# Optimization experiments

Hardware: AMD Instinct MI355X
Metric: run time of the kernel (lower is better)

Reference implementation:

```python
import jax, jax.numpy as jnp
import numpy as np

B, H, W, C = 32, 56, 56, 512
WS, SHIFT, NH = 7, 3, 16
HID = 4 * C
EPS = 1e-5


def layernorm(x, g, b):
    m = jnp.mean(x, axis=-1, keepdims=True)
    v = jnp.mean(jnp.square(x - m), axis=-1, keepdims=True)
    return (x - m) * jax.lax.rsqrt(v + EPS) * g + b


def setup_inputs() -> dict:
    key = jax.random.key(0)
    ks = jax.random.split(key, 16)
    s = 0.02
    return {
        "x": jax.random.normal(ks[0], (B, H * W, C), jnp.float32),
        "wqkv": jax.random.normal(ks[1], (3 * C, C), jnp.float32) * s,
        "bqkv": jnp.zeros((3 * C,), jnp.float32),
        "wo": jax.random.normal(ks[2], (C, C), jnp.float32) * s,
        "bo": jnp.zeros((C,), jnp.float32),
        "g1": jnp.ones((C,), jnp.float32),
        "b1": jnp.zeros((C,), jnp.float32),
        "g2": jnp.ones((C,), jnp.float32),
        "b2": jnp.zeros((C,), jnp.float32),
        "w_mlp1": jax.random.normal(ks[3], (HID, C), jnp.float32) * s,
        "b_mlp1": jnp.zeros((HID,), jnp.float32),
        "w_mlp2": jax.random.normal(ks[4], (C, HID), jnp.float32) * s,
        "b_mlp2": jnp.zeros((C,), jnp.float32),
    }


def window_partition(x4):
    # (B,H,W,C) -> (B*nW, WS*WS, C)
    x = x4.reshape(B, H // WS, WS, W // WS, WS, C)
    return x.transpose(0, 1, 3, 2, 4, 5).reshape(-1, WS * WS, C)


def window_reverse(win):
    # (B*nW, WS*WS, C) -> (B,H,W,C)
    x = win.reshape(B, H // WS, W // WS, WS, WS, C)
    return x.transpose(0, 1, 3, 2, 4, 5).reshape(B, H, W, C)


def mha(xn, wqkv, bqkv, wo, bo):
    NW, T, _ = xn.shape
    Dh = C // NH
    qkv = xn @ wqkv.T + bqkv                      # (NW, T, 3C)
    q, k, v = jnp.split(qkv, 3, axis=-1)
    sh = lambda t: t.reshape(NW, T, NH, Dh).transpose(0, 2, 1, 3)  # (NW,NH,T,Dh)
    q, k, v = sh(q), sh(k), sh(v)
    scores = jnp.einsum('whqd,whkd->whqk', q, k) * (Dh ** -0.5)
    a = jax.nn.softmax(scores, axis=-1)
    o = jnp.einsum('whqk,whkd->whqd', a, v).transpose(0, 2, 1, 3).reshape(NW, T, C)
    return o @ wo.T + bo


def reference(x, wqkv, bqkv, wo, bo, g1, b1, g2, b2, w_mlp1, b_mlp1, w_mlp2, b_mlp2):
    x4 = x.reshape(B, H, W, C)
    shifted = jnp.roll(x4, (-SHIFT, -SHIFT), axis=(1, 2))
    win = window_partition(shifted)               # (B*64, 49, C)
    shortcut = win
    wn = layernorm(win, g1, b1)
    attn = mha(wn, wqkv, bqkv, wo, bo)
    win = shortcut + attn
    _ = window_reverse(win)  # NOTE: discarded, faithfully matching the source (x is rebuilt from shifted_x)
    xr = jnp.roll(shifted, (SHIFT, SHIFT), axis=(1, 2)).reshape(B, H * W, C)
    h = layernorm(xr, g2, b2)
    h = jax.nn.gelu(h @ w_mlp1.T + b_mlp1, approximate=False) @ w_mlp2.T + b_mlp2
    return xr + h
```

## Files before the change

kernel.cpp:

```cpp
#include <hip/hip_runtime.h>
#include <hip/hip_bf16.h>
#include <cstdint>
#include <cstddef>

#define MROWS 100352
#define CDIM  512
#define HDIM  2048

typedef __attribute__((ext_vector_type(8))) short   short8;
typedef __attribute__((ext_vector_type(8))) __bf16  bf16x8;
typedef __attribute__((ext_vector_type(4))) __bf16  bf16x4;
typedef __attribute__((ext_vector_type(4))) float   floatx4;

static __device__ __forceinline__ unsigned short f2bf(float f) {
  union { float f; unsigned int u; } c; c.f = f;
  unsigned int u = c.u;
  return (unsigned short)((u + 0x7FFFu + ((u >> 16) & 1u)) >> 16);
}

static __device__ __forceinline__ void gload_lds16(const void* g, void* l) {
  __builtin_amdgcn_global_load_lds(
      (const __attribute__((address_space(1))) void*)g,
      (__attribute__((address_space(3))) void*)l, 16, 0, 0);
}

#define BAR()   asm volatile("s_barrier" ::: "memory")
#define LGKM0() asm volatile("s_waitcnt lgkmcnt(0)" ::: "memory")
#define VMC4()  asm volatile("s_waitcnt vmcnt(4)" ::: "memory")
#define VMC0()  asm volatile("s_waitcnt vmcnt(0)" ::: "memory")

__global__ void cast_weights(const float4* __restrict__ s1, unsigned short* __restrict__ d1,
                             const float4* __restrict__ s2, unsigned short* __restrict__ d2) {
  int t = blockIdx.x * 256 + threadIdx.x;
  const int N4 = (HDIM * CDIM) / 4;
  const float4* s; unsigned short* d; int idx;
  if (t < N4) { s = s1; d = d1; idx = t; }
  else        { s = s2; d = d2; idx = t - N4; }
  float4 f = s[idx];
  ushort4 u = make_ushort4(f2bf(f.x), f2bf(f.y), f2bf(f.z), f2bf(f.w));
  *reinterpret_cast<ushort4*>(d + (size_t)idx * 4) = u;
}

__global__ void ln_cast(const float* __restrict__ x, const float* __restrict__ g,
                        const float* __restrict__ b, unsigned short* __restrict__ xn) {
  const int row  = blockIdx.x * 4 + (threadIdx.x >> 6);
  const int lane = threadIdx.x & 63;
  const float4* xr = reinterpret_cast<const float4*>(x + (size_t)row * CDIM);
  const float4 v0 = xr[lane], v1 = xr[lane + 64];
  float s  = v0.x + v0.y + v0.z + v0.w + v1.x + v1.y + v1.z + v1.w;
  float ss = v0.x*v0.x + v0.y*v0.y + v0.z*v0.z + v0.w*v0.w
           + v1.x*v1.x + v1.y*v1.y + v1.z*v1.z + v1.w*v1.w;
#pragma unroll
  for (int o = 1; o < 64; o <<= 1) { s += __shfl_xor(s, o); ss += __shfl_xor(ss, o); }
  const float mean = s * (1.0f / CDIM);
  const float rstd = rsqrtf(ss * (1.0f / CDIM) - mean * mean + 1e-5f);
  const float4* g4 = reinterpret_cast<const float4*>(g);
  const float4* b4 = reinterpret_cast<const float4*>(b);
  const float4 ga = g4[lane], gb = g4[lane + 64];
  const float4 ba = b4[lane], bb = b4[lane + 64];
  ushort4 o0 = make_ushort4(
      f2bf((v0.x - mean) * rstd * ga.x + ba.x),
      f2bf((v0.y - mean) * rstd * ga.y + ba.y),
      f2bf((v0.z - mean) * rstd * ga.z + ba.z),
      f2bf((v0.w - mean) * rstd * ga.w + ba.w));
  ushort4 o1 = make_ushort4(
      f2bf((v1.x - mean) * rstd * gb.x + bb.x),
      f2bf((v1.y - mean) * rstd * gb.y + bb.y),
      f2bf((v1.z - mean) * rstd * gb.z + bb.z),
      f2bf((v1.w - mean) * rstd * gb.w + bb.w));
  unsigned short* orow = xn + (size_t)row * CDIM;
  *reinterpret_cast<ushort4*>(orow + lane * 4)        = o0;
  *reinterpret_cast<ushort4*>(orow + (lane + 64) * 4) = o1;
}

template<int KDIM, int NDIM, int EPI>
__global__ __launch_bounds__(512, 2) void gemm256(
    const unsigned short* __restrict__ A, const unsigned short* __restrict__ Bw,
    const float* __restrict__ bias, const float* __restrict__ resid,
    void* __restrict__ Cout) {
  __shared__ __align__(16) unsigned short sm[2][2][2][8192];

  const int tid  = threadIdx.x;
  const int lane = tid & 63, w = tid >> 6;
  const int swr = w >> 2, swc = w & 3;
  const int frow = tid & 15, fk = ((tid & 63) >> 4) * 8;

  constexpr int GX = NDIM / 256;
  const int nwg = gridDim.x;
  const int lid = ((int)blockIdx.x & 7) * (nwg >> 3) + ((int)blockIdx.x >> 3);
  const int m0 = (lid / GX) * 256, n0 = (lid % GX) * 256;

  const size_t ldb = (size_t)KDIM * 2;
  const int srow = tid >> 3;
  const int scb  = ((tid ^ (tid >> 3)) & 7) * 16;
  const char* gA = (const char*)A  + (size_t)(m0 + srow) * ldb + scb;
  const char* gB = (const char*)Bw + (size_t)(n0 + srow) * ldb + scb;

  auto STG = [&](const char* gbase, int tile, int half, int isB) {
    unsigned short* hb = &sm[isB][tile & 1][half][0];
    const char* s = gbase + (size_t)half * 128 * ldb + (size_t)tile * 128;
    gload_lds16(s,            hb + w * 512);
    gload_lds16(s + 64 * ldb, hb + 4096 + w * 512);
  };
  auto LDA = [&](bf16x8* a, int db, int qm) {
#pragma unroll
    for (int mi = 0; mi < 4; ++mi)
#pragma unroll
      for (int kk = 0; kk < 2; ++kk) {
        const int row = swr * 64 + mi * 16 + frow;
        const int col = kk * 32 + fk;
        const int sidx = row * 64 + (col ^ ((row & 7) << 3));
        a[mi * 2 + kk] = __builtin_bit_cast(bf16x8,
            *reinterpret_cast<const short8*>(&sm[0][db][qm][sidx]));
      }
  };
  auto LDBf = [&](bf16x8* b, int db, int qn) {
#pragma unroll
    for (int nj = 0; nj < 2; ++nj)
#pragma unroll
      for (int kk = 0; kk < 2; ++kk) {
        const int row = swc * 32 + nj * 16 + frow;
        const int col = kk * 32 + fk;
        const int sidx = row * 64 + (col ^ ((row & 7) << 3));
        b[nj * 2 + kk] = __builtin_bit_cast(bf16x8,
            *reinterpret_cast<const short8*>(&sm[1][db][qn][sidx]));
      }
  };

  floatx4 acc[2][2][4][2] = {};
  auto MM = [&](floatx4 (*a2)[2], const bf16x8* a, const bf16x8* b) {
    __builtin_amdgcn_s_setprio(1);
#pragma unroll
    for (int mi = 0; mi < 4; ++mi)
#pragma unroll
      for (int nj = 0; nj < 2; ++nj)
#pragma unroll
        for (int kk = 0; kk < 2; ++kk)
          a2[mi][nj] = __builtin_amdgcn_mfma_f32_16x16x32_bf16(
              b[nj * 2 + kk], a[mi * 2 + kk], a2[mi][nj], 0, 0, 0);
    __builtin_amdgcn_s_setprio(0);
  };

  constexpr int nt = KDIM / 64;

  STG(gA, 0, 0, 0); STG(gB, 0, 0, 1);
  STG(gA, 0, 1, 0); STG(gB, 0, 1, 1);
  STG(gA, 1, 0, 0); STG(gB, 1, 0, 1);
  VMC4();
  BAR();

  for (int t2 = 0; t2 < nt; ++t2) {
    const int db = t2 & 1;
    bf16x8 a[8], b0[4], b1[4];

    LDA(a, db, 0); LDBf(b0, db, 0);
    if (t2 + 1 < nt) STG(gA, t2 + 1, 1, 0);
    BAR(); LGKM0();
    MM(acc[0][0], a, b0);
    BAR();

    LDBf(b1, db, 1);
    if (t2 + 1 < nt) STG(gB, t2 + 1, 1, 1);
    BAR(); LGKM0();
    MM(acc[0][1], a, b1);
    BAR();

    LDA(a, db, 1);
    if (t2 + 2 < nt) STG(gA, t2 + 2, 0, 0);
    BAR(); LGKM0();
    MM(acc[1][0], a, b0);
    BAR();

    if (t2 + 2 < nt) STG(gB, t2 + 2, 0, 1);
    BAR(); LGKM0();
    MM(acc[1][1], a, b1);
    if (t2 < nt - 2)       { VMC4(); }
    else if (t2 == nt - 2) { VMC0(); }
    BAR();
  }

  const int em = lane & 15;
  const int en = (lane >> 4) << 2;

  float4 bj[4];
#pragma unroll
  for (int qn = 0; qn < 2; ++qn)
#pragma unroll
    for (int nj = 0; nj < 2; ++nj)
      bj[qn * 2 + nj] = *reinterpret_cast<const float4*>(
          &bias[n0 + qn * 128 + swc * 32 + nj * 16 + en]);

#pragma unroll
  for (int qm = 0; qm < 2; ++qm)
#pragma unroll
    for (int mi = 0; mi < 4; ++mi) {
      const int gm = m0 + qm * 128 + swr * 64 + mi * 16 + em;
      const size_t rowoff = (size_t)gm * NDIM + n0 + swc * 32 + en;
#pragma unroll
      for (int qn = 0; qn < 2; ++qn)
#pragma unroll
        for (int nj = 0; nj < 2; ++nj) {
          const float4 bb = bj[qn * 2 + nj];
          const floatx4 av = acc[qm][qn][mi][nj];
          float v0 = av[0] + bb.x, v1 = av[1] + bb.y;
          float v2 = av[2] + bb.z, v3 = av[3] + bb.w;
          const size_t off = rowoff + qn * 128 + nj * 16;
          if (EPI == 1) {
            v0 *= __builtin_amdgcn_rcpf(1.0f + __expf(-1.702f * v0));
            v1 *= __builtin_amdgcn_rcpf(1.0f + __expf(-1.702f * v1));
            v2 *= __builtin_amdgcn_rcpf(1.0f + __expf(-1.702f * v2));
            v3 *= __builtin_amdgcn_rcpf(1.0f + __expf(-1.702f * v3));
            bf16x4 o = { (__bf16)v0, (__bf16)v1, (__bf16)v2, (__bf16)v3 };
            *reinterpret_cast<bf16x4*>((unsigned short*)Cout + off) = o;
          } else {
            const float4 r4 = *reinterpret_cast<const float4*>(resid + off);
            float4 o = make_float4(v0 + r4.x, v1 + r4.y, v2 + r4.z, v3 + r4.w);
            *reinterpret_cast<float4*>((float*)Cout + off) = o;
          }
        }
    }
}

extern "C" void kernel_launch(void* const* d_in, const int* in_sizes, int n_in,
                              void* d_out, int out_size, void* d_ws, size_t ws_size,
                              hipStream_t stream) {
  const float* x   = (const float*)d_in[0];
  const float* g2  = (const float*)d_in[7];
  const float* b2  = (const float*)d_in[8];
  const float* w1  = (const float*)d_in[9];
  const float* b1  = (const float*)d_in[10];
  const float* w2  = (const float*)d_in[11];
  const float* b2m = (const float*)d_in[12];
  float* out = (float*)d_out;


  unsigned short* w1b = (unsigned short*)d_ws;
  unsigned short* w2b = w1b + (size_t)HDIM * CDIM;
  unsigned short* G   = w2b + (size_t)HDIM * CDIM;
  unsigned short* xn = (unsigned short*)d_out;

  cast_weights<<<2048, 256, 0, stream>>>((const float4*)w1, w1b, (const float4*)w2, w2b);
  ln_cast<<<MROWS / 4, 256, 0, stream>>>(x, g2, b2, xn);

  gemm256<CDIM, HDIM, 1><<<dim3((HDIM / 256) * (MROWS / 256)), 512, 0, stream>>>(
      xn, w1b, b1, nullptr, (void*)G);
  gemm256<HDIM, CDIM, 2><<<dim3((CDIM / 256) * (MROWS / 256)), 512, 0, stream>>>(
      G, w2b, b2m, x, (void*)out);
}
```

Baseline: 643.8 us.

## Replace quarter-split GEMM pipeline with simple double-buffered templated tile kernel

Swaps the hand-interleaved four-quadrant GEMM schedule, which had staged loads, barriers and partial vmcnt waits, for a plain double-buffered loop. Each iteration prefetches the next full K-tile and computes the current one, then waits for all loads and syncs once. The kernel is now templated on BN and the warp grid, and the second GEMM uses 256x128 tiles with a 4x2 warp layout, doubling its workgroup count. The simpler schedule drops the fine-grained overlap and needs more registers for larger fragment sets, in exchange for fewer barriers.

```diff
diff --git a/kernel.cpp b/kernel.cpp
--- a/kernel.cpp
+++ b/kernel.cpp
@@ -25,8 +25,6 @@
 }
 
 #define BAR()   asm volatile("s_barrier" ::: "memory")
-#define LGKM0() asm volatile("s_waitcnt lgkmcnt(0)" ::: "memory")
-#define VMC4()  asm volatile("s_waitcnt vmcnt(4)" ::: "memory")
 #define VMC0()  asm volatile("s_waitcnt vmcnt(0)" ::: "memory")
 
 __global__ void cast_weights(const float4* __restrict__ s1, unsigned short* __restrict__ d1,
@@ -73,22 +71,30 @@
   *reinterpret_cast<ushort4*>(orow + (lane + 64) * 4) = o1;
 }
 
-template<int KDIM, int NDIM, int EPI>
-__global__ __launch_bounds__(512, 2) void gemm256(
+template<int KDIM, int NDIM, int BN, int WGM, int WGN, int EPI>
+__global__ __launch_bounds__(512, 2) void gemm_pipe(
     const unsigned short* __restrict__ A, const unsigned short* __restrict__ Bw,
     const float* __restrict__ bias, const float* __restrict__ resid,
     void* __restrict__ Cout) {
-  __shared__ __align__(16) unsigned short sm[2][2][2][8192];
+  constexpr int BM   = 256;
+  constexpr int WM   = BM / WGM;
+  constexpr int WN   = BN / WGN;
+  constexpr int AM16 = WM / 16;
+  constexpr int AN16 = WN / 16;
+  constexpr int nt   = KDIM / 64;
+
+  __shared__ __align__(16) unsigned short smA[2][BM * 64];
+  __shared__ __align__(16) unsigned short smB[2][BN * 64];
 
   const int tid  = threadIdx.x;
   const int lane = tid & 63, w = tid >> 6;
-  const int swr = w >> 2, swc = w & 3;
-  const int frow = tid & 15, fk = ((tid & 63) >> 4) * 8;
-
-  constexpr int GX = NDIM / 256;
+  const int swr = w / WGN, swc = w % WGN;
+  const int frow = lane & 15, fk = (lane >> 4) * 8;
+
+  constexpr int GX = NDIM / BN;
   const int nwg = gridDim.x;
   const int lid = ((int)blockIdx.x & 7) * (nwg >> 3) + ((int)blockIdx.x >> 3);
-  const int m0 = (lid / GX) * 256, n0 = (lid % GX) * 256;
+  const int m0 = (lid / GX) * BM, n0 = (lid % GX) * BN;
 
   const size_t ldb = (size_t)KDIM * 2;
   const int srow = tid >> 3;
@@ -96,129 +102,100 @@
   const char* gA = (const char*)A  + (size_t)(m0 + srow) * ldb + scb;
   const char* gB = (const char*)Bw + (size_t)(n0 + srow) * ldb + scb;
 
-  auto STG = [&](const char* gbase, int tile, int half, int isB) {
-    unsigned short* hb = &sm[isB][tile & 1][half][0];
-    const char* s = gbase + (size_t)half * 128 * ldb + (size_t)tile * 128;
-    gload_lds16(s,            hb + w * 512);
-    gload_lds16(s + 64 * ldb, hb + 4096 + w * 512);
+  auto STG = [&](int t, int buf) {
+    const char* sa = gA + (size_t)t * 128;
+    const char* sb = gB + (size_t)t * 128;
+#pragma unroll
+    for (int j = 0; j < BM / 64; ++j)
+      gload_lds16(sa + (size_t)j * 64 * ldb, &smA[buf][j * 4096 + w * 512]);
+#pragma unroll
+    for (int j = 0; j < BN / 64; ++j)
+      gload_lds16(sb + (size_t)j * 64 * ldb, &smB[buf][j * 4096 + w * 512]);
   };
-  auto LDA = [&](bf16x8* a, int db, int qm) {
-#pragma unroll
-    for (int mi = 0; mi < 4; ++mi)
+
+  floatx4 acc[AM16][AN16] = {};
+
+  STG(0, 0);
+  VMC0();
+  BAR();
+
+  for (int t = 0; t < nt; ++t) {
+    const int r = t & 1;
+    if (t + 1 < nt) STG(t + 1, r ^ 1);
+
+    bf16x8 bfr[AN16 * 2], afr[AM16 * 2];
+#pragma unroll
+    for (int nj = 0; nj < AN16; ++nj)
 #pragma unroll
       for (int kk = 0; kk < 2; ++kk) {
-        const int row = swr * 64 + mi * 16 + frow;
+        const int row = swc * WN + nj * 16 + frow;
         const int col = kk * 32 + fk;
-        const int sidx = row * 64 + (col ^ ((row & 7) << 3));
-        a[mi * 2 + kk] = __builtin_bit_cast(bf16x8,
-            *reinterpret_cast<const short8*>(&sm[0][db][qm][sidx]));
+        bfr[nj * 2 + kk] = __builtin_bit_cast(bf16x8,
+            *reinterpret_cast<const short8*>(
+                &smB[r][row * 64 + (col ^ ((row & 7) << 3))]));
       }
-  };
-  auto LDBf = [&](bf16x8* b, int db, int qn) {
-#pragma unroll
-    for (int nj = 0; nj < 2; ++nj)
+#pragma unroll
+    for (int mi = 0; mi < AM16; ++mi)
 #pragma unroll
       for (int kk = 0; kk < 2; ++kk) {
-        const int row = swc * 32 + nj * 16 + frow;
+        const int row = swr * WM + mi * 16 + frow;
         const int col = kk * 32 + fk;
-        const int sidx = row * 64 + (col ^ ((row & 7) << 3));
-        b[nj * 2 + kk] = __builtin_bit_cast(bf16x8,
-            *reinterpret_cast<const short8*>(&sm[1][db][qn][sidx]));
+        afr[mi * 2 + kk] = __builtin_bit_cast(bf16x8,
+            *reinterpret_cast<const short8*>(
+                &smA[r][row * 64 + (col ^ ((row & 7) << 3))]));
       }
-  };
-
-  floatx4 acc[2][2][4][2] = {};
-  auto MM = [&](floatx4 (*a2)[2], const bf16x8* a, const bf16x8* b) {
+
     __builtin_amdgcn_s_setprio(1);
 #pragma unroll
-    for (int mi = 0; mi < 4; ++mi)
-#pragma unroll
-      for (int nj = 0; nj < 2; ++nj)
+    for (int mi = 0; mi < AM16; ++mi)
+#pragma unroll
+      for (int nj = 0; nj < AN16; ++nj)
 #pragma unroll
         for (int kk = 0; kk < 2; ++kk)
-          a2[mi][nj] = __builtin_amdgcn_mfma_f32_16x16x32_bf16(
-              b[nj * 2 + kk], a[mi * 2 + kk], a2[mi][nj], 0, 0, 0);
+          acc[mi][nj] = __builtin_amdgcn_mfma_f32_16x16x32_bf16(
+              bfr[nj * 2 + kk], afr[mi * 2 + kk], acc[mi][nj], 0, 0, 0);
     __builtin_amdgcn_s_setprio(0);
-  };
-
-  constexpr int nt = KDIM / 64;
-
-  STG(gA, 0, 0, 0); STG(gB, 0, 0, 1);
-  STG(gA, 0, 1, 0); STG(gB, 0, 1, 1);
-  STG(gA, 1, 0, 0); STG(gB, 1, 0, 1);
-  VMC4();
-  BAR();
-
-  for (int t2 = 0; t2 < nt; ++t2) {
-    const int db = t2 & 1;
-    bf16x8 a[8], b0[4], b1[4];
-
-    LDA(a, db, 0); LDBf(b0, db, 0);
-    if (t2 + 1 < nt) STG(gA, t2 + 1, 1, 0);
-    BAR(); LGKM0();
-    MM(acc[0][0], a, b0);
-    BAR();
-
-    LDBf(b1, db, 1);
-    if (t2 + 1 < nt) STG(gB, t2 + 1, 1, 1);
-    BAR(); LGKM0();
-    MM(acc[0][1], a, b1);
-    BAR();
-
-    LDA(a, db, 1);
-    if (t2 + 2 < nt) STG(gA, t2 + 2, 0, 0);
-    BAR(); LGKM0();
-    MM(acc[1][0], a, b0);
-    BAR();
-
-    if (t2 + 2 < nt) STG(gB, t2 + 2, 0, 1);
-    BAR(); LGKM0();
-    MM(acc[1][1], a, b1);
-    if (t2 < nt - 2)       { VMC4(); }
-    else if (t2 == nt - 2) { VMC0(); }
-    BAR();
+
+    if (t + 1 < nt) {
+      VMC0();
+      BAR();
+    }
   }
 
   const int em = lane & 15;
   const int en = (lane >> 4) << 2;
 
-  float4 bj[4];
-#pragma unroll
-  for (int qn = 0; qn < 2; ++qn)
-#pragma unroll
-    for (int nj = 0; nj < 2; ++nj)
-      bj[qn * 2 + nj] = *reinterpret_cast<const float4*>(
-          &bias[n0 + qn * 128 + swc * 32 + nj * 16 + en]);
-
-#pragma unroll
-  for (int qm = 0; qm < 2; ++qm)
-#pragma unroll
-    for (int mi = 0; mi < 4; ++mi) {
-      const int gm = m0 + qm * 128 + swr * 64 + mi * 16 + em;
-      const size_t rowoff = (size_t)gm * NDIM + n0 + swc * 32 + en;
-#pragma unroll
-      for (int qn = 0; qn < 2; ++qn)
-#pragma unroll
-        for (int nj = 0; nj < 2; ++nj) {
-          const float4 bb = bj[qn * 2 + nj];
-          const floatx4 av = acc[qm][qn][mi][nj];
-          float v0 = av[0] + bb.x, v1 = av[1] + bb.y;
-          float v2 = av[2] + bb.z, v3 = av[3] + bb.w;
-          const size_t off = rowoff + qn * 128 + nj * 16;
-          if (EPI == 1) {
-            v0 *= __builtin_amdgcn_rcpf(1.0f + __expf(-1.702f * v0));
-            v1 *= __builtin_amdgcn_rcpf(1.0f + __expf(-1.702f * v1));
-            v2 *= __builtin_amdgcn_rcpf(1.0f + __expf(-1.702f * v2));
-            v3 *= __builtin_amdgcn_rcpf(1.0f + __expf(-1.702f * v3));
-            bf16x4 o = { (__bf16)v0, (__bf16)v1, (__bf16)v2, (__bf16)v3 };
-            *reinterpret_cast<bf16x4*>((unsigned short*)Cout + off) = o;
-          } else {
-            const float4 r4 = *reinterpret_cast<const float4*>(resid + off);
-            float4 o = make_float4(v0 + r4.x, v1 + r4.y, v2 + r4.z, v3 + r4.w);
-            *reinterpret_cast<float4*>((float*)Cout + off) = o;
-          }
-        }
+  float4 bj[AN16];
+#pragma unroll
+  for (int nj = 0; nj < AN16; ++nj)
+    bj[nj] = *reinterpret_cast<const float4*>(&bias[n0 + swc * WN + nj * 16 + en]);
+
+#pragma unroll
+  for (int mi = 0; mi < AM16; ++mi) {
+    const int gm = m0 + swr * WM + mi * 16 + em;
+    const size_t rowoff = (size_t)gm * NDIM + n0 + swc * WN + en;
+#pragma unroll
+    for (int nj = 0; nj < AN16; ++nj) {
+      const float4 bb = bj[nj];
+      const floatx4 av = acc[mi][nj];
+      const size_t off = rowoff + nj * 16;
+      if (EPI == 1) {
+        float v0 = av[0] + bb.x, v1 = av[1] + bb.y;
+        float v2 = av[2] + bb.z, v3 = av[3] + bb.w;
+        v0 *= __builtin_amdgcn_rcpf(1.0f + __expf(-1.702f * v0));
+        v1 *= __builtin_amdgcn_rcpf(1.0f + __expf(-1.702f * v1));
+        v2 *= __builtin_amdgcn_rcpf(1.0f + __expf(-1.702f * v2));
+        v3 *= __builtin_amdgcn_rcpf(1.0f + __expf(-1.702f * v3));
+        bf16x4 o = { (__bf16)v0, (__bf16)v1, (__bf16)v2, (__bf16)v3 };
+        *reinterpret_cast<bf16x4*>((unsigned short*)Cout + off) = o;
+      } else {
+        const float4 r4 = *reinterpret_cast<const float4*>(resid + off);
+        float4 o = make_float4(av[0] + bb.x + r4.x, av[1] + bb.y + r4.y,
+                               av[2] + bb.z + r4.z, av[3] + bb.w + r4.w);
+        *reinterpret_cast<float4*>((float*)Cout + off) = o;
+      }
     }
+  }
 }
 
 extern "C" void kernel_launch(void* const* d_in, const int* in_sizes, int n_in,
@@ -242,8 +219,11 @@
   cast_weights<<<2048, 256, 0, stream>>>((const float4*)w1, w1b, (const float4*)w2, w2b);
   ln_cast<<<MROWS / 4, 256, 0, stream>>>(x, g2, b2, xn);
 
-  gemm256<CDIM, HDIM, 1><<<dim3((HDIM / 256) * (MROWS / 256)), 512, 0, stream>>>(
-      xn, w1b, b1, nullptr, (void*)G);
-  gemm256<HDIM, CDIM, 2><<<dim3((CDIM / 256) * (MROWS / 256)), 512, 0, stream>>>(
-      G, w2b, b2m, x, (void*)out);
-}
+  gemm_pipe<CDIM, HDIM, 256, 2, 4, 1>
+      <<<dim3((MROWS / 256) * (HDIM / 256)), 512, 0, stream>>>(
+          xn, w1b, b1, nullptr, (void*)G);
+
+  gemm_pipe<HDIM, CDIM, 128, 4, 2, 2>
+      <<<dim3((MROWS / 256) * (CDIM / 128)), 512, 0, stream>>>(
+          G, w2b, b2m, x, (void*)out);
+}
```

New measurement: 826.2 us. +28.3%, slower.

## Restructure GEMM main loop to load all fragments upfront and cut barriers

Applied to the files above, without the earlier changes.

The K-loop now loads both A halves and both B halves from LDS at the start of each iteration, issues the next-stage global-to-LDS copies, and runs all four MFMA blocks with only one or two barriers instead of eight. Launch bounds drop to one block per CU so the extra fragment registers (a0 and a1) fit without spilling. The aim is to remove barrier stalls and overlap LDS reads with MFMA work, at the cost of lower occupancy and higher register pressure. Correctness depends on the reduced barrier placement still guarding LDS buffer reuse.

```diff
diff --git a/kernel.cpp b/kernel.cpp
--- a/kernel.cpp
+++ b/kernel.cpp
@@ -74,7 +74,7 @@
 }
 
 template<int KDIM, int NDIM, int EPI>
-__global__ __launch_bounds__(512, 2) void gemm256(
+__global__ __launch_bounds__(512, 1) void gemm256(
     const unsigned short* __restrict__ A, const unsigned short* __restrict__ Bw,
     const float* __restrict__ bias, const float* __restrict__ resid,
     void* __restrict__ Cout) {
@@ -149,34 +149,30 @@
   VMC4();
   BAR();
 
-  for (int t2 = 0; t2 < nt; ++t2) {
-    const int db = t2 & 1;
-    bf16x8 a[8], b0[4], b1[4];
-
-    LDA(a, db, 0); LDBf(b0, db, 0);
-    if (t2 + 1 < nt) STG(gA, t2 + 1, 1, 0);
-    BAR(); LGKM0();
-    MM(acc[0][0], a, b0);
-    BAR();
-
-    LDBf(b1, db, 1);
-    if (t2 + 1 < nt) STG(gB, t2 + 1, 1, 1);
-    BAR(); LGKM0();
-    MM(acc[0][1], a, b1);
-    BAR();
-
-    LDA(a, db, 1);
-    if (t2 + 2 < nt) STG(gA, t2 + 2, 0, 0);
-    BAR(); LGKM0();
-    MM(acc[1][0], a, b0);
-    BAR();
-
-    if (t2 + 2 < nt) STG(gB, t2 + 2, 0, 1);
-    BAR(); LGKM0();
-    MM(acc[1][1], a, b1);
-    if (t2 < nt - 2)       { VMC4(); }
-    else if (t2 == nt - 2) { VMC0(); }
-    BAR();
+  for (int t = 0; t < nt; ++t) {
+    const int db = t & 1;
+    bf16x8 a0[8], a1[8], b0[4], b1[4];
+
+    LDA(a0, db, 0); LDBf(b0, db, 0);
+    LDBf(b1, db, 1); LDA(a1, db, 1);
+
+    if (t + 1 < nt) { STG(gA, t + 1, 1, 0); STG(gB, t + 1, 1, 1); }
+
+    MM(acc[0][0], a0, b0);
+    MM(acc[0][1], a0, b1);
+
+    if (t + 2 < nt) {
+      LGKM0();
+      BAR();
+      STG(gA, t + 2, 0, 0);
+      STG(gB, t + 2, 0, 1);
+    }
+
+    MM(acc[1][0], a1, b0);
+    MM(acc[1][1], a1, b1);
+
+    if (t + 2 < nt)      { VMC4(); BAR(); }
+    else if (t + 1 < nt) { VMC0(); BAR(); }
   }
 
   const int em = lane & 15;
```

After: 643.0 us. No clear change (-0.1%).
